# Kernel tuning notes

Measured on AMD Instinct MI355X. Metric: run time of the kernel, lower is better.

The kernel has to match this reference:

```python
import jax, jax.numpy as jnp
import numpy as np

KRYLOV_DIM = 8
T_END = 1.0
EPS = 1e-12


def setup_inputs() -> dict:
    key = jax.random.key(0)
    k1, k2, k3 = jax.random.split(key, 3)
    B, C, H, Wd = 8, 256, 64, 64
    s0 = jax.random.uniform(k1, (B, C, H, Wd), dtype=jnp.float32)
    v = jax.random.normal(k2, (B, C, H, Wd), dtype=jnp.float32)
    W = jax.random.normal(k3, (C, C), dtype=jnp.float32) / np.float32(np.sqrt(C))
    return {"s0": s0, "v": v, "W": W}


def reference(s0, v, W):
    # fitness: learned channel-mixing linear operator (1x1-conv style)
    def fitness(x):
        return jnp.einsum('oc,bchw->bohw', W, x)

    # replicator vector field R_{s}[x] = s*x - s * sum_c(s*x)
    def replicator(s, x):
        sx = s * x
        return sx - s * jnp.sum(sx, axis=1, keepdims=True)

    A = lambda x: fitness(replicator(s0, x))
    dot = lambda a, b: jnp.sum(a * b, axis=(1, 2, 3))  # batched inner product

    m = KRYLOV_DIM
    B = v.shape[0]

    # ---- Arnoldi iteration (batched, modified Gram-Schmidt) ----
    vnorm = jnp.sqrt(dot(v, v))  # [B]
    Q = [v / vnorm[:, None, None, None]]
    Hcols = []
    for k in range(m):
        w = A(Q[k])
        col = []
        for j in range(k + 1):
            h = dot(Q[j], w)               # [B]
            col.append(h)
            w = w - h[:, None, None, None] * Q[j]
        hnext = jnp.sqrt(dot(w, w))        # subdiagonal entry
        Q.append(w / (hnext + EPS)[:, None, None, None])
        col.append(hnext)
        col += [jnp.zeros_like(hnext)] * (m - k - 1)  # pad column to m+1 rows
        Hcols.append(jnp.stack(col, axis=-1))          # [B, m+1]
    Hmat = jnp.stack(Hcols, axis=-1)  # [B, m+1, m]
    T = Hmat[:, :m, :]                # square upper-Hessenberg [B, m, m]

    # ---- extended matrix + batched small matrix exponential ----
    ext = jnp.zeros((B, m + 1, m + 1), dtype=T.dtype)
    ext = ext.at[:, :m, :m].set(T_END * T)
    ext = ext.at[:, 0, m].set(T_END)
    expm_ext = jax.scipy.linalg.expm(ext)   # batched over leading dim
    coords = expm_ext[:, :m, -1]            # [B, m] Krylov coordinates

    # ---- fused weighted sum of Krylov vectors ----
    Qstack = jnp.stack(Q[:m], axis=0)       # [m, B, C, H, W]
    v_end = jnp.einsum('bj,jbchw->bchw', coords, Qstack)
    return v_end * vnorm[:, None, None, None]
```

## Files before the change

kernel.cpp:

```cpp
#include <hip/hip_runtime.h>
#include <math.h>

#define Bn   8
#define Cn   256
#define HWn  4096
#define FB   (Cn * HWn)
#define NTOT (Bn * FB)
#define TEND 1.0
#define EPSK 1e-12f
#define NT   64
#define TSZ  16384
#define RS   40
#define WTS  68

typedef float f32x4 __attribute__((ext_vector_type(4)));
typedef short bf16x8 __attribute__((ext_vector_type(8)));

__device__ inline float b2f(unsigned int u) {
    return __uint_as_float(u << 16);
}
__device__ inline unsigned short f2b(float f) {
    unsigned u = __float_as_uint(f);
    unsigned r = u + 0x7FFFu + ((u >> 16) & 1u);
    return (unsigned short)(r >> 16);
}


__global__ void init_kernel(float* __restrict__ p) {
    for (int i = threadIdx.x; i < 1024; i += 256) p[i] = 0.0f;
}

__global__ void wsplit_kernel(const float* __restrict__ W,
                              unsigned short* __restrict__ Whs,
                              unsigned short* __restrict__ Wls) {
    int kc = blockIdx.x, mt = blockIdx.y, l = threadIdx.x;
    int m = mt * 16 + (l & 15);
    int k0 = kc * 32 + (l >> 4) * 8;
#pragma unroll
    for (int j = 0; j < 8; ++j) {
        float wv = W[m * 256 + k0 + j];
        unsigned short h = f2b(wv);
        unsigned short lo = f2b(wv - b2f(h));
        int idx = ((kc * 16 + mt) * 64 + l) * 8 + j;
        Whs[idx] = h; Wls[idx] = lo;
    }
}

__global__ __launch_bounds__(256) void relayout_kernel(const float* __restrict__ src,
                                                       float* __restrict__ dst) {
    int t = blockIdx.x, b = blockIdx.y;
    const size_t sb = (size_t)b * FB;
    const size_t db = ((size_t)b * 64 + t) * TSZ;
    int cg = threadIdx.x >> 4;
    int pos4 = (threadIdx.x & 15) * 4;
#pragma unroll
    for (int ci = 0; ci < 16; ++ci) {
        int c = ci * 16 + cg;
        float4 x = *(const float4*)(src + sb + (size_t)c * HWn + t * NT + pos4);
        *(float4*)(dst + db + c * 64 + pos4) = x;
    }
}

template <int K>
__global__ __launch_bounds__(512, 2) void step_kernel(
        const float* __restrict__ v, const float* __restrict__ s0t,
        const unsigned short* __restrict__ Whs, const unsigned short* __restrict__ Wls,
        unsigned short* __restrict__ Qb, float* __restrict__ acc,
        float* __restrict__ w) {
    __shared__ __align__(16) char smem_u[69632];
    short* Pbuf[2][2];
    short* Sbuf[2][2];
    Pbuf[0][0] = (short*)smem_u;                 Pbuf[0][1] = (short*)(smem_u + 5120);
    Pbuf[1][0] = (short*)(smem_u + 10240);       Pbuf[1][1] = (short*)(smem_u + 15360);
    Sbuf[0][0] = (short*)(smem_u + 20480);       Sbuf[0][1] = (short*)(smem_u + 25600);
    Sbuf[1][0] = (short*)(smem_u + 30720);       Sbuf[1][1] = (short*)(smem_u + 35840);
    float* tredf = (float*)smem_u;
    float* wt    = (float*)smem_u;
    __shared__ float ts[NT];
    __shared__ float nred[8];
    __shared__ float dred[8][8];

    const int tid = threadIdx.x;
    const int lane = tid & 63, wvi = tid >> 6;
    const int b = blockIdx.y;
    const int tIdx = blockIdx.x;
    const int sbase = tIdx * NT;
    const size_t boff = (size_t)b * FB;
    const size_t tbase = ((size_t)b * 64 + tIdx) * TSZ;
    const int mbase = wvi * 32;
    const int cch = tid >> 4;
    const int pos4 = (tid & 15) * 4;
    const int codd = cch & 1;
    const int c2s = cch >> 1;

    float cj[K > 0 ? K : 1];
    if (K > 0) {
        float mm[K > 0 ? K : 1];
        mm[0] = sqrtf(acc[512 + b]);
#pragma unroll
        for (int j = 1; j < K; ++j) mm[j] = sqrtf(acc[512 + j * 8 + b]) + EPSK * mm[j - 1];
#pragma unroll
        for (int j = 0; j < K; ++j)
            cj[j] = acc[((K - 1) * 8 + j) * 8 + b] / (mm[j] * mm[j]);
    }
    unsigned short* QK = Qb + (size_t)(K > 0 ? K - 1 : 0) * NTOT;

    float tp[4] = {0.f, 0.f, 0.f, 0.f};
    float np = 0.f;

    auto wr2 = [&](short* buf, unsigned x01, unsigned x23) {
        unsigned p01 = (unsigned)__shfl_xor((int)x01, 16);
        unsigned p23 = (unsigned)__shfl_xor((int)x23, 16);
        unsigned mine = codd ? x23 : x01;
        unsigned theirs = codd ? p23 : p01;
        unsigned w0, w1;
        if (codd) {
            w0 = (theirs & 0xFFFFu) | (mine << 16);
            w1 = (theirs >> 16) | (mine & 0xFFFF0000u);
        } else {
            w0 = (mine & 0xFFFFu) | (theirs << 16);
            w1 = (mine >> 16) | (theirs & 0xFFFF0000u);
        }
        int P0 = pos4 + 2 * codd;
        int slot = c2s ^ (((P0 >> 3) & 3) << 2);
        *(unsigned*)(buf + P0 * RS + slot * 2) = w0;
        *(unsigned*)(buf + (P0 + 1) * RS + slot * 2) = w1;
    };

    struct Ld {
        float4 s4, w4, v4;
        ushort4 q[K > 1 ? K - 1 : 1];
    };
    auto issue = [&](int kc) -> Ld {
        Ld L;
        const size_t oe = tbase + (size_t)((kc * 32 + cch) * 64 + pos4);
        const size_t ov = boff + (size_t)(kc * 32 + cch) * HWn + sbase + pos4;
        L.s4 = *(const float4*)(s0t + oe);
        if (K == 0) {
            L.v4 = *(const float4*)(v + ov);
        } else {
            L.w4 = *(const float4*)(w + oe);
            L.v4 = *(const float4*)(v + ov);
#pragma unroll
            for (int j = 1; j < K; ++j)
                L.q[j - 1] = *(const ushort4*)(Qb + (size_t)(j - 1) * NTOT + oe);
        }
        return L;
    };
    auto consume = [&](Ld& L, int kc, int bb) {
        const size_t oe = tbase + (size_t)((kc * 32 + cch) * 64 + pos4);
        float se[4] = {L.s4.x, L.s4.y, L.s4.z, L.s4.w};
        float xr[4];
        if (K == 0) {
            xr[0] = L.v4.x; xr[1] = L.v4.y; xr[2] = L.v4.z; xr[3] = L.v4.w;
        } else {
            float xe[4];
            xe[0] = fmaf(-cj[0], L.v4.x, L.w4.x);
            xe[1] = fmaf(-cj[0], L.v4.y, L.w4.y);
            xe[2] = fmaf(-cj[0], L.v4.z, L.w4.z);
            xe[3] = fmaf(-cj[0], L.v4.w, L.w4.w);
#pragma unroll
            for (int j = 1; j < K; ++j) {
                xe[0] = fmaf(-cj[j], b2f(L.q[j - 1].x), xe[0]);
                xe[1] = fmaf(-cj[j], b2f(L.q[j - 1].y), xe[1]);
                xe[2] = fmaf(-cj[j], b2f(L.q[j - 1].z), xe[2]);
                xe[3] = fmaf(-cj[j], b2f(L.q[j - 1].w), xe[3]);
            }
            unsigned h0 = f2b(xe[0]), h1 = f2b(xe[1]);
            unsigned h2 = f2b(xe[2]), h3 = f2b(xe[3]);
            ushort4 o;
            o.x = (unsigned short)h0; o.y = (unsigned short)h1;
            o.z = (unsigned short)h2; o.w = (unsigned short)h3;
            *(ushort4*)(QK + oe) = o;
            xr[0] = b2f(h0); xr[1] = b2f(h1); xr[2] = b2f(h2); xr[3] = b2f(h3);
        }
        unsigned phx[4], plx[4], shx[4], slx[4];
#pragma unroll
        for (int i = 0; i < 4; ++i) {
            np = fmaf(xr[i], xr[i], np);
            tp[i] = fmaf(xr[i], se[i], tp[i]);
            float pe = se[i] * xr[i];
            unsigned hp = f2b(pe);
            phx[i] = hp; plx[i] = f2b(pe - b2f((unsigned short)hp));
            unsigned hs = f2b(se[i]);
            shx[i] = hs; slx[i] = f2b(se[i] - b2f((unsigned short)hs));
        }
        wr2(Pbuf[0][bb], phx[0] | (phx[1] << 16), phx[2] | (phx[3] << 16));
        wr2(Pbuf[1][bb], plx[0] | (plx[1] << 16), plx[2] | (plx[3] << 16));
        wr2(Sbuf[0][bb], shx[0] | (shx[1] << 16), shx[2] | (shx[3] << 16));
        wr2(Sbuf[1][bb], slx[0] | (slx[1] << 16), slx[2] | (slx[3] << 16));
    };

    f32x4 ac[2][4], az[2][4];
#pragma unroll
    for (int i = 0; i < 2; ++i)
#pragma unroll
        for (int j = 0; j < 4; ++j) {
            ac[i][j] = (f32x4){0.f, 0.f, 0.f, 0.f};
            az[i][j] = (f32x4){0.f, 0.f, 0.f, 0.f};
        }

    const int r15 = lane & 15, qq = lane >> 4;
    {
        Ld L0 = issue(0);
        consume(L0, 0, 0);
    }
    for (int kc = 0; kc < 8; ++kc) {
        __syncthreads();
        bf16x8 ah[2], al[2];
#pragma unroll
        for (int rt = 0; rt < 2; ++rt) {
            int mt = (mbase >> 4) + rt;
            ah[rt] = *(const bf16x8*)(Whs + (size_t)kc * 8192 + (mt * 64 + lane) * 8);
            al[rt] = *(const bf16x8*)(Wls + (size_t)kc * 8192 + (mt * 64 + lane) * 8);
        }
        Ld Ln;
        if (kc < 7) Ln = issue(kc + 1);
        const short* ph = Pbuf[0][kc & 1];
        const short* pl = Pbuf[1][kc & 1];
        const short* sh = Sbuf[0][kc & 1];
        const short* sl = Sbuf[1][kc & 1];
#pragma unroll
        for (int ct = 0; ct < 4; ++ct) {
            int n = ct * 16 + r15;
            int grp = qq ^ ((n >> 3) & 3);
            int off = n * RS + grp * 8;
            bf16x8 bh = *(const bf16x8*)(ph + off);
            bf16x8 bl = *(const bf16x8*)(pl + off);
            bf16x8 svh = *(const bf16x8*)(sh + off);
            bf16x8 svl = *(const bf16x8*)(sl + off);
#pragma unroll
            for (int rt = 0; rt < 2; ++rt) {
                ac[rt][ct] = __builtin_amdgcn_mfma_f32_16x16x32_bf16(ah[rt], bh, ac[rt][ct], 0, 0, 0);
                ac[rt][ct] = __builtin_amdgcn_mfma_f32_16x16x32_bf16(ah[rt], bl, ac[rt][ct], 0, 0, 0);
                ac[rt][ct] = __builtin_amdgcn_mfma_f32_16x16x32_bf16(al[rt], bh, ac[rt][ct], 0, 0, 0);
                az[rt][ct] = __builtin_amdgcn_mfma_f32_16x16x32_bf16(ah[rt], svh, az[rt][ct], 0, 0, 0);
                az[rt][ct] = __builtin_amdgcn_mfma_f32_16x16x32_bf16(ah[rt], svl, az[rt][ct], 0, 0, 0);
                az[rt][ct] = __builtin_amdgcn_mfma_f32_16x16x32_bf16(al[rt], svh, az[rt][ct], 0, 0, 0);
            }
        }
        if (kc < 7) consume(Ln, kc + 1, (kc + 1) & 1);
    }

    __syncthreads();
    *(float4*)(tredf + cch * WTS + pos4) = *(float4*)tp;
    {
        float q2 = np;
        for (int off2 = 32; off2 > 0; off2 >>= 1) q2 += __shfl_down(q2, off2);
        if (lane == 0) nred[wvi] = q2;
    }
    __syncthreads();
    if (tid < NT) {
        float s = 0.f;
#pragma unroll
        for (int g = 0; g < 32; ++g) s += tredf[g * WTS + tid];
        ts[tid] = s;
    }
    if (tid == 0)
        atomicAdd(&acc[512 + K * 8 + b],
                  nred[0] + nred[1] + nred[2] + nred[3] +
                  nred[4] + nred[5] + nred[6] + nred[7]);
    __syncthreads();

#pragma unroll
    for (int rt = 0; rt < 2; ++rt)
#pragma unroll
        for (int ct = 0; ct < 4; ++ct) {
            int col = ct * 16 + r15;
            int r0 = mbase + rt * 16 + qq * 4;
            float tv = ts[col];
#pragma unroll
            for (int reg = 0; reg < 4; ++reg)
                wt[(r0 + reg) * WTS + col] = ac[rt][ct][reg] - az[rt][ct][reg] * tv;
        }
    __syncthreads();

    float dp[K + 1];
#pragma unroll
    for (int j = 0; j <= K; ++j) dp[j] = 0.f;
#pragma unroll
    for (int rr = 0; rr < 8; ++rr) {
        int row = rr * 32 + (tid >> 4);
        int col = (tid & 15) * 4;
        float4 wv4 = *(const float4*)(wt + row * WTS + col);
        size_t ide = tbase + (size_t)(row * 64 + col);
        *(float4*)(w + ide) = wv4;
        float4 vv4 = *(const float4*)(v + boff + (size_t)row * HWn + sbase + col);
        dp[0] = fmaf(wv4.x, vv4.x, dp[0]);
        dp[0] = fmaf(wv4.y, vv4.y, dp[0]);
        dp[0] = fmaf(wv4.z, vv4.z, dp[0]);
        dp[0] = fmaf(wv4.w, vv4.w, dp[0]);
#pragma unroll
        for (int j = 1; j <= K; ++j) {
            ushort4 u = *(const ushort4*)(Qb + (size_t)(j - 1) * NTOT + ide);
            dp[j] = fmaf(wv4.x, b2f(u.x), dp[j]);
            dp[j] = fmaf(wv4.y, b2f(u.y), dp[j]);
            dp[j] = fmaf(wv4.z, b2f(u.z), dp[j]);
            dp[j] = fmaf(wv4.w, b2f(u.w), dp[j]);
        }
    }
#pragma unroll
    for (int j = 0; j <= K; ++j) {
        float q2 = dp[j];
        for (int off2 = 32; off2 > 0; off2 >>= 1) q2 += __shfl_down(q2, off2);
        if (lane == 0) dred[wvi][j] = q2;
    }
    __syncthreads();
    if (tid <= K)
        atomicAdd(&acc[(K * 8 + tid) * 8 + b],
                  dred[0][tid] + dred[1][tid] + dred[2][tid] + dred[3][tid] +
                  dred[4][tid] + dred[5][tid] + dred[6][tid] + dred[7][tid]);
}

__global__ __launch_bounds__(128) void expm_kernel(const float* __restrict__ acc,
                                                   float* __restrict__ coordsOut) {
    __shared__ double Am[81], Pm[81], Tm[81];
    __shared__ double ssc;
    __shared__ int sn;
    const int b = blockIdx.x;
    const int t = threadIdx.x;
    const int r = t / 9, c = t % 9;
    double m[8];
    m[0] = sqrt((double)acc[512 + b]);
    for (int j = 1; j < 8; ++j) m[j] = sqrt((double)acc[512 + j * 8 + b]) + 1e-12 * m[j - 1];
    if (t < 81) {
        double val = 0.0;
        if (r < 8 && c < 8) {
            if (r <= c) val = TEND * (double)acc[(c * 8 + r) * 8 + b] / (m[r] * m[c]);
            else if (r == c + 1) val = TEND * sqrt((double)acc[512 + r * 8 + b]) / m[c];
        }
        if (r == 0 && c == 8) val = TEND;
        Am[t] = val;
    }
    __syncthreads();
    if (t == 0) {
        double mx = 0.0;
        for (int rr = 0; rr < 9; ++rr) {
            double s = 0.0;
            for (int cc = 0; cc < 9; ++cc) s += fabs(Am[rr * 9 + cc]);
            if (s > mx) mx = s;
        }
        int n = 0;
        while (mx > 0.25 && n < 48) { mx *= 0.5; ++n; }
        double sc = 1.0;
        for (int ii = 0; ii < n; ++ii) sc *= 0.5;
        sn = n; ssc = sc;
    }
    __syncthreads();
    if (t < 81) Am[t] *= ssc;
    __syncthreads();
    if (t < 81) Pm[t] = (r == c) ? 1.0 : 0.0;
    __syncthreads();
    for (int i = 20; i >= 1; --i) {
        if (t < 81) {
            double s = 0.0;
            for (int k = 0; k < 9; ++k) s += Am[r * 9 + k] * Pm[k * 9 + c];
            Tm[t] = ((r == c) ? 1.0 : 0.0) + s / (double)i;
        }
        __syncthreads();
        if (t < 81) Pm[t] = Tm[t];
        __syncthreads();
    }
    int n = sn;
    for (int q = 0; q < n; ++q) {
        if (t < 81) {
            double s = 0.0;
            for (int k = 0; k < 9; ++k) s += Pm[r * 9 + k] * Pm[k * 9 + c];
            Tm[t] = s;
        }
        __syncthreads();
        if (t < 81) Pm[t] = Tm[t];
        __syncthreads();
    }
    if (t < 8) coordsOut[b * 8 + t] = (float)(Pm[t * 9 + 8] * m[0] / m[t]);
}

__global__ __launch_bounds__(256) void combine_kernel(const unsigned short* __restrict__ Qb,
                                                      const float* __restrict__ v,
                                                      const float* __restrict__ coords,
                                                      float* __restrict__ out) {
    int t = blockIdx.x, b = blockIdx.y;
    const size_t boff = (size_t)b * FB;
    const size_t tb = ((size_t)b * 64 + t) * TSZ;
    float cf[8];
#pragma unroll
    for (int j = 0; j < 8; ++j) cf[j] = coords[b * 8 + j];
    int rg = threadIdx.x >> 4;
    int pos4 = (threadIdx.x & 15) * 4;
#pragma unroll
    for (int ri = 0; ri < 16; ++ri) {
        int r = ri * 16 + rg;
        size_t ti = tb + (size_t)(r * 64 + pos4);
        size_t si = boff + (size_t)r * HWn + t * NT + pos4;
        float4 vv = *(const float4*)(v + si);
        float a[4] = {cf[0] * vv.x, cf[0] * vv.y, cf[0] * vv.z, cf[0] * vv.w};
#pragma unroll
        for (int j = 1; j < 8; ++j) {
            ushort4 u = *(const ushort4*)(Qb + (size_t)(j - 1) * NTOT + ti);
            a[0] = fmaf(cf[j], b2f(u.x), a[0]);
            a[1] = fmaf(cf[j], b2f(u.y), a[1]);
            a[2] = fmaf(cf[j], b2f(u.z), a[2]);
            a[3] = fmaf(cf[j], b2f(u.w), a[3]);
        }
        float4 o = {a[0], a[1], a[2], a[3]};
        *(float4*)(out + si) = o;
    }
}

extern "C" void kernel_launch(void* const* d_in, const int* in_sizes, int n_in,
                              void* d_out, int out_size, void* d_ws, size_t ws_size,
                              hipStream_t stream) {
    const float* s0 = (const float*)d_in[0];
    const float* v  = (const float*)d_in[1];
    const float* W  = (const float*)d_in[2];
    float* out = (float*)d_out;

    float* ws     = (float*)d_ws;
    float* acc    = ws;
    float* coords = ws + 576;
    unsigned short* Whs = (unsigned short*)(ws + 1024);
    unsigned short* Wls = Whs + 65536;
    float* s0t    = ws + 1024 + 65536;
    unsigned short* Qb = (unsigned short*)(s0t + NTOT);
    float* w      = out;

    init_kernel<<<dim3(1), dim3(256), 0, stream>>>(ws);
    wsplit_kernel<<<dim3(8, 16), dim3(64), 0, stream>>>(W, Whs, Wls);
    relayout_kernel<<<dim3(64, 8), dim3(256), 0, stream>>>(s0, s0t);

    dim3 ga(64, 8), blk(512);
#define STEPK(K) step_kernel<K><<<ga, blk, 0, stream>>>(v, s0t, Whs, Wls, Qb, acc, w);
    STEPK(0) STEPK(1) STEPK(2) STEPK(3) STEPK(4) STEPK(5) STEPK(6) STEPK(7)
#undef STEPK

    expm_kernel<<<dim3(8), dim3(128), 0, stream>>>(acc, coords);
    combine_kernel<<<dim3(64, 8), dim3(256), 0, stream>>>(Qb, v, coords, out);
}
```

Baseline: 567.6 us.

## Precompute W·s0 once and halve per-step MFMA work with smaller tiles

The replicator term W·(s0·sum) is split out: a new K=-1 pass computes Z = W·s0 once and stores it as a bf16 hi/lo pair, so each of the eight step kernels only runs the W·(s0∘x) GEMM and subtracts Z scaled by the per-pixel sum. This removes half of the MFMAs and the s0 bf16 split/LDS traffic in every step, at the cost of one extra GEMM pass and reading Zh/Zl per step. Tiles shrink to 32 pixels with 256-thread blocks (4 blocks/CU), and the s0 relayout kernel is dropped in favour of reading s0 directly.

```diff
diff --git a/kernel.cpp b/kernel.cpp
--- a/kernel.cpp
+++ b/kernel.cpp
@@ -8,10 +8,11 @@
 #define NTOT (Bn * FB)
 #define TEND 1.0
 #define EPSK 1e-12f
-#define NT   64
-#define TSZ  16384
+#define NT   32
+#define TPB  128
+#define TSZ  8192
 #define RS   40
-#define WTS  68
+#define WTS  36
 
 typedef float f32x4 __attribute__((ext_vector_type(4)));
 typedef short bf16x8 __attribute__((ext_vector_type(8)));
@@ -46,39 +47,23 @@
     }
 }
 
-__global__ __launch_bounds__(256) void relayout_kernel(const float* __restrict__ src,
-                                                       float* __restrict__ dst) {
-    int t = blockIdx.x, b = blockIdx.y;
-    const size_t sb = (size_t)b * FB;
-    const size_t db = ((size_t)b * 64 + t) * TSZ;
-    int cg = threadIdx.x >> 4;
-    int pos4 = (threadIdx.x & 15) * 4;
-#pragma unroll
-    for (int ci = 0; ci < 16; ++ci) {
-        int c = ci * 16 + cg;
-        float4 x = *(const float4*)(src + sb + (size_t)c * HWn + t * NT + pos4);
-        *(float4*)(dst + db + c * 64 + pos4) = x;
-    }
-}
-
 template <int K>
-__global__ __launch_bounds__(512, 2) void step_kernel(
-        const float* __restrict__ v, const float* __restrict__ s0t,
+__global__ __launch_bounds__(256, 4) void step_kernel(
+        const float* __restrict__ v, const float* __restrict__ s0,
         const unsigned short* __restrict__ Whs, const unsigned short* __restrict__ Wls,
         unsigned short* __restrict__ Qb, float* __restrict__ acc,
-        float* __restrict__ w) {
-    __shared__ __align__(16) char smem_u[69632];
-    short* Pbuf[2][2];
-    short* Sbuf[2][2];
-    Pbuf[0][0] = (short*)smem_u;                 Pbuf[0][1] = (short*)(smem_u + 5120);
-    Pbuf[1][0] = (short*)(smem_u + 10240);       Pbuf[1][1] = (short*)(smem_u + 15360);
-    Sbuf[0][0] = (short*)(smem_u + 20480);       Sbuf[0][1] = (short*)(smem_u + 25600);
-    Sbuf[1][0] = (short*)(smem_u + 30720);       Sbuf[1][1] = (short*)(smem_u + 35840);
-    float* tredf = (float*)smem_u;
+        float* __restrict__ w,
+        unsigned short* __restrict__ Zh, unsigned short* __restrict__ Zl) {
+    __shared__ __align__(16) char smem_u[36864];
+    short* Ph0 = (short*)smem_u;
+    short* Ph1 = (short*)(smem_u + 2560);
+    short* Pl0 = (short*)(smem_u + 5120);
+    short* Pl1 = (short*)(smem_u + 7680);
+    float* tredf = (float*)(smem_u + 10240);
     float* wt    = (float*)smem_u;
     __shared__ float ts[NT];
-    __shared__ float nred[8];
-    __shared__ float dred[8][8];
+    __shared__ float nred[4];
+    __shared__ float dred[4][8];
 
     const int tid = threadIdx.x;
     const int lane = tid & 63, wvi = tid >> 6;
@@ -86,10 +71,10 @@
     const int tIdx = blockIdx.x;
     const int sbase = tIdx * NT;
     const size_t boff = (size_t)b * FB;
-    const size_t tbase = ((size_t)b * 64 + tIdx) * TSZ;
-    const int mbase = wvi * 32;
-    const int cch = tid >> 4;
-    const int pos4 = (tid & 15) * 4;
+    const size_t tb = ((size_t)b * TPB + tIdx) * TSZ;
+    const int mbase = wvi * 64;
+    const int cch = tid >> 3;
+    const int pos4 = (tid & 7) * 4;
     const int codd = cch & 1;
     const int c2s = cch >> 1;
 
@@ -109,8 +94,8 @@
     float np = 0.f;
 
     auto wr2 = [&](short* buf, unsigned x01, unsigned x23) {
-        unsigned p01 = (unsigned)__shfl_xor((int)x01, 16);
-        unsigned p23 = (unsigned)__shfl_xor((int)x23, 16);
+        unsigned p01 = (unsigned)__shfl_xor((int)x01, 8);
+        unsigned p23 = (unsigned)__shfl_xor((int)x23, 8);
         unsigned mine = codd ? x23 : x01;
         unsigned theirs = codd ? p23 : p01;
         unsigned w0, w1;
@@ -133,27 +118,27 @@
     };
     auto issue = [&](int kc) -> Ld {
         Ld L;
-        const size_t oe = tbase + (size_t)((kc * 32 + cch) * 64 + pos4);
-        const size_t ov = boff + (size_t)(kc * 32 + cch) * HWn + sbase + pos4;
-        L.s4 = *(const float4*)(s0t + oe);
+        const size_t os = boff + (size_t)(kc * 32 + cch) * HWn + sbase + pos4;
+        const size_t ot = tb + (size_t)((kc * 32 + cch) * NT + pos4);
+        L.s4 = *(const float4*)(s0 + os);
         if (K == 0) {
-            L.v4 = *(const float4*)(v + ov);
-        } else {
-            L.w4 = *(const float4*)(w + oe);
-            L.v4 = *(const float4*)(v + ov);
+            L.v4 = *(const float4*)(v + os);
+        } else if (K > 0) {
+            L.w4 = *(const float4*)(w + ot);
+            L.v4 = *(const float4*)(v + os);
 #pragma unroll
             for (int j = 1; j < K; ++j)
-                L.q[j - 1] = *(const ushort4*)(Qb + (size_t)(j - 1) * NTOT + oe);
+                L.q[j - 1] = *(const ushort4*)(Qb + (size_t)(j - 1) * NTOT + ot);
         }
         return L;
     };
     auto consume = [&](Ld& L, int kc, int bb) {
-        const size_t oe = tbase + (size_t)((kc * 32 + cch) * 64 + pos4);
+        const size_t ot = tb + (size_t)((kc * 32 + cch) * NT + pos4);
         float se[4] = {L.s4.x, L.s4.y, L.s4.z, L.s4.w};
-        float xr[4];
+        float xr[4] = {0.f, 0.f, 0.f, 0.f};
         if (K == 0) {
             xr[0] = L.v4.x; xr[1] = L.v4.y; xr[2] = L.v4.z; xr[3] = L.v4.w;
-        } else {
+        } else if (K > 0) {
             float xe[4];
             xe[0] = fmaf(-cj[0], L.v4.x, L.w4.x);
             xe[1] = fmaf(-cj[0], L.v4.y, L.w4.y);
@@ -171,34 +156,32 @@
             ushort4 o;
             o.x = (unsigned short)h0; o.y = (unsigned short)h1;
             o.z = (unsigned short)h2; o.w = (unsigned short)h3;
-            *(ushort4*)(QK + oe) = o;
+            *(ushort4*)(QK + ot) = o;
             xr[0] = b2f(h0); xr[1] = b2f(h1); xr[2] = b2f(h2); xr[3] = b2f(h3);
         }
-        unsigned phx[4], plx[4], shx[4], slx[4];
+        unsigned phx[4], plx[4];
 #pragma unroll
         for (int i = 0; i < 4; ++i) {
-            np = fmaf(xr[i], xr[i], np);
-            tp[i] = fmaf(xr[i], se[i], tp[i]);
-            float pe = se[i] * xr[i];
+            float pe;
+            if (K < 0) {
+                pe = se[i];
+            } else {
+                np = fmaf(xr[i], xr[i], np);
+                tp[i] = fmaf(xr[i], se[i], tp[i]);
+                pe = se[i] * xr[i];
+            }
             unsigned hp = f2b(pe);
             phx[i] = hp; plx[i] = f2b(pe - b2f((unsigned short)hp));
-            unsigned hs = f2b(se[i]);
-            shx[i] = hs; slx[i] = f2b(se[i] - b2f((unsigned short)hs));
-        }
-        wr2(Pbuf[0][bb], phx[0] | (phx[1] << 16), phx[2] | (phx[3] << 16));
-        wr2(Pbuf[1][bb], plx[0] | (plx[1] << 16), plx[2] | (plx[3] << 16));
-        wr2(Sbuf[0][bb], shx[0] | (shx[1] << 16), shx[2] | (shx[3] << 16));
-        wr2(Sbuf[1][bb], slx[0] | (slx[1] << 16), slx[2] | (slx[3] << 16));
+        }
+        wr2(bb ? Ph1 : Ph0, phx[0] | (phx[1] << 16), phx[2] | (phx[3] << 16));
+        wr2(bb ? Pl1 : Pl0, plx[0] | (plx[1] << 16), plx[2] | (plx[3] << 16));
     };
 
-    f32x4 ac[2][4], az[2][4];
-#pragma unroll
-    for (int i = 0; i < 2; ++i)
-#pragma unroll
-        for (int j = 0; j < 4; ++j) {
-            ac[i][j] = (f32x4){0.f, 0.f, 0.f, 0.f};
-            az[i][j] = (f32x4){0.f, 0.f, 0.f, 0.f};
-        }
+    f32x4 ac[4][2];
+#pragma unroll
+    for (int i = 0; i < 4; ++i)
+#pragma unroll
+        for (int j = 0; j < 2; ++j) ac[i][j] = (f32x4){0.f, 0.f, 0.f, 0.f};
 
     const int r15 = lane & 15, qq = lane >> 4;
     {
@@ -207,109 +190,123 @@
     }
     for (int kc = 0; kc < 8; ++kc) {
         __syncthreads();
-        bf16x8 ah[2], al[2];
-#pragma unroll
-        for (int rt = 0; rt < 2; ++rt) {
-            int mt = (mbase >> 4) + rt;
+        bf16x8 ah[4], al[4];
+#pragma unroll
+        for (int rt = 0; rt < 4; ++rt) {
+            int mt = wvi * 4 + rt;
             ah[rt] = *(const bf16x8*)(Whs + (size_t)kc * 8192 + (mt * 64 + lane) * 8);
             al[rt] = *(const bf16x8*)(Wls + (size_t)kc * 8192 + (mt * 64 + lane) * 8);
         }
         Ld Ln;
         if (kc < 7) Ln = issue(kc + 1);
-        const short* ph = Pbuf[0][kc & 1];
-        const short* pl = Pbuf[1][kc & 1];
-        const short* sh = Sbuf[0][kc & 1];
-        const short* sl = Sbuf[1][kc & 1];
-#pragma unroll
-        for (int ct = 0; ct < 4; ++ct) {
+        const short* ph = (kc & 1) ? Ph1 : Ph0;
+        const short* pl = (kc & 1) ? Pl1 : Pl0;
+#pragma unroll
+        for (int ct = 0; ct < 2; ++ct) {
             int n = ct * 16 + r15;
             int grp = qq ^ ((n >> 3) & 3);
             int off = n * RS + grp * 8;
             bf16x8 bh = *(const bf16x8*)(ph + off);
             bf16x8 bl = *(const bf16x8*)(pl + off);
-            bf16x8 svh = *(const bf16x8*)(sh + off);
-            bf16x8 svl = *(const bf16x8*)(sl + off);
-#pragma unroll
-            for (int rt = 0; rt < 2; ++rt) {
+#pragma unroll
+            for (int rt = 0; rt < 4; ++rt) {
                 ac[rt][ct] = __builtin_amdgcn_mfma_f32_16x16x32_bf16(ah[rt], bh, ac[rt][ct], 0, 0, 0);
                 ac[rt][ct] = __builtin_amdgcn_mfma_f32_16x16x32_bf16(ah[rt], bl, ac[rt][ct], 0, 0, 0);
                 ac[rt][ct] = __builtin_amdgcn_mfma_f32_16x16x32_bf16(al[rt], bh, ac[rt][ct], 0, 0, 0);
-                az[rt][ct] = __builtin_amdgcn_mfma_f32_16x16x32_bf16(ah[rt], svh, az[rt][ct], 0, 0, 0);
-                az[rt][ct] = __builtin_amdgcn_mfma_f32_16x16x32_bf16(ah[rt], svl, az[rt][ct], 0, 0, 0);
-                az[rt][ct] = __builtin_amdgcn_mfma_f32_16x16x32_bf16(al[rt], svh, az[rt][ct], 0, 0, 0);
             }
         }
         if (kc < 7) consume(Ln, kc + 1, (kc + 1) & 1);
     }
 
     __syncthreads();
-    *(float4*)(tredf + cch * WTS + pos4) = *(float4*)tp;
-    {
+    if (K >= 0) {
+        *(float4*)(tredf + cch * WTS + pos4) = *(float4*)tp;
         float q2 = np;
         for (int off2 = 32; off2 > 0; off2 >>= 1) q2 += __shfl_down(q2, off2);
         if (lane == 0) nred[wvi] = q2;
     }
     __syncthreads();
-    if (tid < NT) {
-        float s = 0.f;
-#pragma unroll
-        for (int g = 0; g < 32; ++g) s += tredf[g * WTS + tid];
-        ts[tid] = s;
-    }
-    if (tid == 0)
-        atomicAdd(&acc[512 + K * 8 + b],
-                  nred[0] + nred[1] + nred[2] + nred[3] +
-                  nred[4] + nred[5] + nred[6] + nred[7]);
-    __syncthreads();
-
-#pragma unroll
-    for (int rt = 0; rt < 2; ++rt)
-#pragma unroll
-        for (int ct = 0; ct < 4; ++ct) {
+    if (K >= 0) {
+        if (tid < NT) {
+            float s = 0.f;
+#pragma unroll
+            for (int g = 0; g < 32; ++g) s += tredf[g * WTS + tid];
+            ts[tid] = s;
+        }
+        if (tid == 0)
+            atomicAdd(&acc[512 + K * 8 + b], nred[0] + nred[1] + nred[2] + nred[3]);
+    }
+    __syncthreads();
+
+#pragma unroll
+    for (int rt = 0; rt < 4; ++rt)
+#pragma unroll
+        for (int ct = 0; ct < 2; ++ct) {
             int col = ct * 16 + r15;
             int r0 = mbase + rt * 16 + qq * 4;
-            float tv = ts[col];
 #pragma unroll
             for (int reg = 0; reg < 4; ++reg)
-                wt[(r0 + reg) * WTS + col] = ac[rt][ct][reg] - az[rt][ct][reg] * tv;
-        }
-    __syncthreads();
-
-    float dp[K + 1];
-#pragma unroll
-    for (int j = 0; j <= K; ++j) dp[j] = 0.f;
+                wt[(r0 + reg) * WTS + col] = ac[rt][ct][reg];
+        }
+    __syncthreads();
+
+    float dp[K >= 0 ? K + 1 : 1];
+#pragma unroll
+    for (int j = 0; j < (K >= 0 ? K + 1 : 1); ++j) dp[j] = 0.f;
 #pragma unroll
     for (int rr = 0; rr < 8; ++rr) {
-        int row = rr * 32 + (tid >> 4);
-        int col = (tid & 15) * 4;
+        int row = rr * 32 + (tid >> 3);
+        int col = (tid & 7) * 4;
         float4 wv4 = *(const float4*)(wt + row * WTS + col);
-        size_t ide = tbase + (size_t)(row * 64 + col);
-        *(float4*)(w + ide) = wv4;
-        float4 vv4 = *(const float4*)(v + boff + (size_t)row * HWn + sbase + col);
-        dp[0] = fmaf(wv4.x, vv4.x, dp[0]);
-        dp[0] = fmaf(wv4.y, vv4.y, dp[0]);
-        dp[0] = fmaf(wv4.z, vv4.z, dp[0]);
-        dp[0] = fmaf(wv4.w, vv4.w, dp[0]);
-#pragma unroll
-        for (int j = 1; j <= K; ++j) {
-            ushort4 u = *(const ushort4*)(Qb + (size_t)(j - 1) * NTOT + ide);
-            dp[j] = fmaf(wv4.x, b2f(u.x), dp[j]);
-            dp[j] = fmaf(wv4.y, b2f(u.y), dp[j]);
-            dp[j] = fmaf(wv4.z, b2f(u.z), dp[j]);
-            dp[j] = fmaf(wv4.w, b2f(u.w), dp[j]);
-        }
-    }
-#pragma unroll
-    for (int j = 0; j <= K; ++j) {
-        float q2 = dp[j];
-        for (int off2 = 32; off2 > 0; off2 >>= 1) q2 += __shfl_down(q2, off2);
-        if (lane == 0) dred[wvi][j] = q2;
-    }
-    __syncthreads();
-    if (tid <= K)
-        atomicAdd(&acc[(K * 8 + tid) * 8 + b],
-                  dred[0][tid] + dred[1][tid] + dred[2][tid] + dred[3][tid] +
-                  dred[4][tid] + dred[5][tid] + dred[6][tid] + dred[7][tid]);
+        size_t it = tb + (size_t)(row * NT + col);
+        if (K < 0) {
+            ushort4 zh4, zl4;
+            unsigned short h0 = f2b(wv4.x), h1 = f2b(wv4.y);
+            unsigned short h2 = f2b(wv4.z), h3 = f2b(wv4.w);
+            zh4.x = h0; zh4.y = h1; zh4.z = h2; zh4.w = h3;
+            zl4.x = f2b(wv4.x - b2f(h0)); zl4.y = f2b(wv4.y - b2f(h1));
+            zl4.z = f2b(wv4.z - b2f(h2)); zl4.w = f2b(wv4.w - b2f(h3));
+            *(ushort4*)(Zh + it) = zh4;
+            *(ushort4*)(Zl + it) = zl4;
+        } else {
+            size_t is = boff + (size_t)row * HWn + sbase + col;
+            ushort4 zh4 = *(const ushort4*)(Zh + it);
+            ushort4 zl4 = *(const ushort4*)(Zl + it);
+            float z0 = b2f(zh4.x) + b2f(zl4.x), z1 = b2f(zh4.y) + b2f(zl4.y);
+            float z2 = b2f(zh4.z) + b2f(zl4.z), z3 = b2f(zh4.w) + b2f(zl4.w);
+            float4 wf;
+            wf.x = wv4.x - z0 * ts[col + 0];
+            wf.y = wv4.y - z1 * ts[col + 1];
+            wf.z = wv4.z - z2 * ts[col + 2];
+            wf.w = wv4.w - z3 * ts[col + 3];
+            *(float4*)(w + it) = wf;
+            float4 vv4 = *(const float4*)(v + is);
+            dp[0] = fmaf(wf.x, vv4.x, dp[0]);
+            dp[0] = fmaf(wf.y, vv4.y, dp[0]);
+            dp[0] = fmaf(wf.z, vv4.z, dp[0]);
+            dp[0] = fmaf(wf.w, vv4.w, dp[0]);
+#pragma unroll
+            for (int j = 1; j <= (K >= 0 ? K : 0); ++j) {
+                ushort4 u = *(const ushort4*)(Qb + (size_t)(j - 1) * NTOT + it);
+                dp[j] = fmaf(wf.x, b2f(u.x), dp[j]);
+                dp[j] = fmaf(wf.y, b2f(u.y), dp[j]);
+                dp[j] = fmaf(wf.z, b2f(u.z), dp[j]);
+                dp[j] = fmaf(wf.w, b2f(u.w), dp[j]);
+            }
+        }
+    }
+    if (K >= 0) {
+#pragma unroll
+        for (int j = 0; j <= K; ++j) {
+            float q2 = dp[j];
+            for (int off2 = 32; off2 > 0; off2 >>= 1) q2 += __shfl_down(q2, off2);
+            if (lane == 0) dred[wvi][j] = q2;
+        }
+        __syncthreads();
+        if (tid <= K)
+            atomicAdd(&acc[(K * 8 + tid) * 8 + b],
+                      dred[0][tid] + dred[1][tid] + dred[2][tid] + dred[3][tid]);
+    }
 }
 
 __global__ __launch_bounds__(128) void expm_kernel(const float* __restrict__ acc,
@@ -381,29 +378,29 @@
                                                       float* __restrict__ out) {
     int t = blockIdx.x, b = blockIdx.y;
     const size_t boff = (size_t)b * FB;
-    const size_t tb = ((size_t)b * 64 + t) * TSZ;
+    const size_t tb = ((size_t)b * TPB + t) * TSZ;
     float cf[8];
 #pragma unroll
     for (int j = 0; j < 8; ++j) cf[j] = coords[b * 8 + j];
-    int rg = threadIdx.x >> 4;
-    int pos4 = (threadIdx.x & 15) * 4;
-#pragma unroll
-    for (int ri = 0; ri < 16; ++ri) {
-        int r = ri * 16 + rg;
-        size_t ti = tb + (size_t)(r * 64 + pos4);
-        size_t si = boff + (size_t)r * HWn + t * NT + pos4;
-        float4 vv = *(const float4*)(v + si);
+    int rg = threadIdx.x >> 3;
+    int pos4 = (threadIdx.x & 7) * 4;
+#pragma unroll
+    for (int ri = 0; ri < 8; ++ri) {
+        int r = ri * 32 + rg;
+        size_t it = tb + (size_t)(r * NT + pos4);
+        size_t is = boff + (size_t)r * HWn + t * NT + pos4;
+        float4 vv = *(const float4*)(v + is);
         float a[4] = {cf[0] * vv.x, cf[0] * vv.y, cf[0] * vv.z, cf[0] * vv.w};
 #pragma unroll
         for (int j = 1; j < 8; ++j) {
-            ushort4 u = *(const ushort4*)(Qb + (size_t)(j - 1) * NTOT + ti);
+            ushort4 u = *(const ushort4*)(Qb + (size_t)(j - 1) * NTOT + it);
             a[0] = fmaf(cf[j], b2f(u.x), a[0]);
             a[1] = fmaf(cf[j], b2f(u.y), a[1]);
             a[2] = fmaf(cf[j], b2f(u.z), a[2]);
             a[3] = fmaf(cf[j], b2f(u.w), a[3]);
         }
         float4 o = {a[0], a[1], a[2], a[3]};
-        *(float4*)(out + si) = o;
+        *(float4*)(out + is) = o;
     }
 }
 
@@ -420,19 +417,20 @@
     float* coords = ws + 576;
     unsigned short* Whs = (unsigned short*)(ws + 1024);
     unsigned short* Wls = Whs + 65536;
-    float* s0t    = ws + 1024 + 65536;
-    unsigned short* Qb = (unsigned short*)(s0t + NTOT);
+    unsigned short* Zh  = (unsigned short*)(ws + 1024 + 65536);
+    unsigned short* Zl  = Zh + NTOT;
+    unsigned short* Qb  = Zh + 2 * (size_t)NTOT;
     float* w      = out;
 
     init_kernel<<<dim3(1), dim3(256), 0, stream>>>(ws);
     wsplit_kernel<<<dim3(8, 16), dim3(64), 0, stream>>>(W, Whs, Wls);
-    relayout_kernel<<<dim3(64, 8), dim3(256), 0, stream>>>(s0, s0t);
-
-    dim3 ga(64, 8), blk(512);
-#define STEPK(K) step_kernel<K><<<ga, blk, 0, stream>>>(v, s0t, Whs, Wls, Qb, acc, w);
+
+    dim3 ga(TPB, 8), blk(256);
+    step_kernel<-1><<<ga, blk, 0, stream>>>(v, s0, Whs, Wls, Qb, acc, w, Zh, Zl);
+#define STEPK(K) step_kernel<K><<<ga, blk, 0, stream>>>(v, s0, Whs, Wls, Qb, acc, w, Zh, Zl);
     STEPK(0) STEPK(1) STEPK(2) STEPK(3) STEPK(4) STEPK(5) STEPK(6) STEPK(7)
 #undef STEPK
 
     expm_kernel<<<dim3(8), dim3(128), 0, stream>>>(acc, coords);
-    combine_kernel<<<dim3(64, 8), dim3(256), 0, stream>>>(Qb, v, coords, out);
-}
+    combine_kernel<<<dim3(TPB, 8), blk, 0, stream>>>(Qb, v, coords, out);
+}
```

Result: slower. 690.2 us (+21.6%).
